# Kernel tuning notes

Hardware: AMD Instinct MI355X
Metric: run time of the kernel (lower is better)

The kernel has to match this reference:

```python
import jax, jax.numpy as jnp
import numpy as np

N_NODES = 100000


def gcn_conv(x, W, b, src, dst, n_nodes):
    """PyG-style GCNConv: add self-loops, symmetric normalization, aggregate to dst."""
    x = x @ W  # [N, out]
    loop = jnp.arange(n_nodes, dtype=src.dtype)
    src_sl = jnp.concatenate([src, loop])  # [E+N]
    dst_sl = jnp.concatenate([dst, loop])
    deg = jax.ops.segment_sum(jnp.ones(src_sl.shape[0], x.dtype), dst_sl,
                              num_segments=n_nodes)  # [N]
    dinv = jnp.where(deg > 0, jax.lax.rsqrt(deg), 0.0)
    norm = dinv[src_sl] * dinv[dst_sl]  # [E+N]
    msg = x[src_sl] * norm[:, None]  # gather + scale
    out = jax.ops.segment_sum(msg, dst_sl, num_segments=n_nodes)  # scatter-add
    return out + b


def setup_inputs() -> dict:
    key = jax.random.key(0)
    ks = jax.random.split(key, 8)
    in_d, hid_d, out_d = 64, 128, 64
    x = jax.random.normal(ks[0], (N_NODES, in_d), dtype=jnp.float32)
    edge_index = jax.random.randint(ks[1], (2, 1000000), 0, N_NODES, dtype=jnp.int64)
    s1 = 1.0 / np.sqrt(in_d)
    s2 = 1.0 / np.sqrt(hid_d)
    sc = 1.0 / np.sqrt(2 * out_d)
    W1 = jax.random.uniform(ks[2], (in_d, hid_d), jnp.float32, -s1, s1)
    b1 = jnp.zeros((hid_d,), jnp.float32)
    W2 = jax.random.uniform(ks[3], (hid_d, out_d), jnp.float32, -s2, s2)
    b2 = jnp.zeros((out_d,), jnp.float32)
    Wc = jax.random.uniform(ks[4], (2 * out_d, 1), jnp.float32, -sc, sc)
    bc = jax.random.uniform(ks[5], (1,), jnp.float32, -sc, sc)
    return {"x": x, "edge_index": edge_index, "W1": W1, "b1": b1,
            "W2": W2, "b2": b2, "Wc": Wc, "bc": bc}


def reference(x, edge_index, W1, b1, W2, b2, Wc, bc):
    src, dst = edge_index[0], edge_index[1]
    h = jax.nn.relu(gcn_conv(x, W1, b1, src, dst, N_NODES))
    h = jax.nn.relu(gcn_conv(h, W2, b2, src, dst, N_NODES))
    # edge-level gather-concat-linear-sigmoid
    edge_emb = jnp.concatenate([h[src], h[dst]], axis=1)  # [E, 2*out_d]
    logits = edge_emb @ Wc + bc  # [E, 1]
    return jax.nn.sigmoid(logits)
```

## Files before the change

### kernel.cpp

```cpp
#include <hip/hip_runtime.h>
#include <hip/hip_fp16.h>
#include <math.h>

#define IN_D 64
#define HID_D 128
#define OUT_D 64

typedef _Float16 half8 __attribute__((ext_vector_type(8)));
typedef float f32x4 __attribute__((ext_vector_type(4)));

#define NBITS  8
#define BNODES 256
#define ECAP   4096
#define CSRCAP (ECAP + BNODES * 7)
#define DCHUNK 2048

__global__ void k_init(int* __restrict__ bcur,
                       const float* __restrict__ W1, const float* __restrict__ W2,
                       __half* __restrict__ w1f, __half* __restrict__ w2f,
                       __half* __restrict__ xs, __half* __restrict__ ts,
                       int N, int nbuk) {
    int t = blockIdx.x * 256 + threadIdx.x;
    if (blockIdx.x == 0) {
        for (int i = threadIdx.x; i < nbuk; i += 256) bcur[i] = i * ECAP;
    }
    if (t < 2048) {
        int which = t >> 10, fl = t & 1023;
        int f = fl >> 6, l = fl & 63, q = l >> 4, n16 = l & 15;
        if (which == 0) {
            int nt = f >> 1, kc = f & 1, n = nt * 16 + n16, k0 = kc * 32 + q * 8;
            for (int j = 0; j < 8; ++j)
                w1f[(size_t)fl * 8 + j] = __float2half(W1[(k0 + j) * 128 + n]);
        } else {
            int nt = f >> 2, kc = f & 3, n = nt * 16 + n16, k0 = kc * 32 + q * 8;
            for (int j = 0; j < 8; ++j)
                w2f[(size_t)fl * 8 + j] = __float2half(W2[(k0 + j) * 64 + n]);
        }
    } else {
        int si = t - 2048;
        if (si < 64) {
            xs[(size_t)N * 64 + si] = __float2half(0.f);
            ts[(size_t)N * 64 + si] = __float2half(0.f);
        }
    }
}

__global__ __launch_bounds__(256) void k_decode3(const unsigned int* __restrict__ raw,
                                                 int E, int nbuk,
                                                 int* __restrict__ bcur,
                                                 int* __restrict__ pairs) {
    __shared__ int hist[512];
    __shared__ int base[512];
    __shared__ int cnt[512];
    __shared__ int is64s;
    if (threadIdx.x == 0) {
        int f = 1;
        for (int i = 1; i < 64; i += 2) f &= (raw[i] == 0u);
        is64s = f;
    }
    for (int i = threadIdx.x; i < nbuk; i += 256) { hist[i] = 0; cnt[i] = 0; }
    __syncthreads();
    int is64 = is64s;
    int e0 = blockIdx.x * DCHUNK;
    int s[8], d[8], b[8];
    if ((E & 1) == 0) {
#pragma unroll
        for (int i = 0; i < 4; ++i) {
            int e = e0 + (threadIdx.x + i * 256) * 2;
            if (e < E) {
                int s0, d0, s1, d1;
                if (is64) {
                    uint4 sv = *(const uint4*)&raw[2 * (size_t)e];
                    uint4 dv = *(const uint4*)&raw[2 * ((size_t)E + e)];
                    s0 = (int)sv.x; s1 = (int)sv.z;
                    d0 = (int)dv.x; d1 = (int)dv.z;
                } else {
                    uint2 sv = *(const uint2*)&raw[e];
                    uint2 dv = *(const uint2*)&raw[E + e];
                    s0 = (int)sv.x; s1 = (int)sv.y;
                    d0 = (int)dv.x; d1 = (int)dv.y;
                }
                s[2 * i] = s0; d[2 * i] = d0; b[2 * i] = d0 >> NBITS;
                s[2 * i + 1] = s1; d[2 * i + 1] = d1; b[2 * i + 1] = d1 >> NBITS;
                atomicAdd(&hist[b[2 * i]], 1);
                atomicAdd(&hist[b[2 * i + 1]], 1);
            } else { b[2 * i] = -1; b[2 * i + 1] = -1; }
        }
    } else {
#pragma unroll
        for (int i = 0; i < 8; ++i) {
            int e = e0 + threadIdx.x + i * 256;
            if (e < E) {
                int sv, dv;
                if (is64) {
                    sv = (int)raw[2 * (size_t)e];
                    dv = (int)raw[2 * ((size_t)E + e)];
                } else {
                    sv = (int)raw[e];
                    dv = (int)raw[E + e];
                }
                s[i] = sv; d[i] = dv; b[i] = dv >> NBITS;
                atomicAdd(&hist[b[i]], 1);
            } else b[i] = -1;
        }
    }
    __syncthreads();
    for (int i = threadIdx.x; i < nbuk; i += 256)
        if (hist[i] > 0) base[i] = atomicAdd(&bcur[i], hist[i]);
    __syncthreads();
#pragma unroll
    for (int i = 0; i < 8; ++i) {
        if (b[i] >= 0) {
            int pos = base[b[i]] + atomicAdd(&cnt[b[i]], 1);
            pairs[pos] = (s[i] << NBITS) | (d[i] & (BNODES - 1));
        }
    }
}

__global__ __launch_bounds__(256) void k_build(const int* __restrict__ pairs,
                                               const int* __restrict__ bcur,
                                               int2* __restrict__ prowdeg,
                                               int* __restrict__ csr_src,
                                               float* __restrict__ dinv,
                                               const float* __restrict__ x,
                                               __half* __restrict__ xs,
                                               int N) {
    __shared__ int deg5[256];
    __shared__ int cur5[256];
    __shared__ int wsum[4];
    int b = blockIdx.x;
    int n0 = b << NBITS;
    int n1 = n0 + BNODES; if (n1 > N) n1 = N;
    int nn = n1 - n0;
    deg5[threadIdx.x] = 0;
    __syncthreads();
    int beg = b * ECAP, end = bcur[b];
    for (int i = beg + threadIdx.x; i < end; i += 256)
        atomicAdd(&deg5[pairs[i] & (BNODES - 1)], 1);
    __syncthreads();
    int pbase = b * CSRCAP;
    int t = threadIdx.x;
    int v0 = deg5[t];
    int p0 = (v0 + 7) & ~7;
    int lane = t & 63, w = t >> 6;
    int inc = p0;
    for (int off = 1; off < 64; off <<= 1) {
        int n = __shfl_up(inc, off);
        if (lane >= off) inc += n;
    }
    if (lane == 63) wsum[w] = inc;
    __syncthreads();
    for (int k = 0; k < w; ++k) inc += wsum[k];
    int ex0 = inc - p0;
    int ps0 = pbase + ex0;
    cur5[t] = ps0;
    if (t < nn) {
        prowdeg[n0 + t] = make_int2(ps0, p0);
        dinv[n0 + t] = rsqrtf((float)v0 + 1.0f);
    }
    __syncthreads();
    for (int i = beg + threadIdx.x; i < end; i += 256) {
        int r = pairs[i];
        int pos = atomicAdd(&cur5[r & (BNODES - 1)], 1);
        csr_src[pos] = r >> NBITS;
    }
    __syncthreads();
    for (int i = cur5[t]; i < ps0 + p0; ++i) csr_src[i] = N;
    for (int idx = t; idx < nn * 8; idx += 256) {
        int i = idx >> 3, c8 = (idx & 7) * 8;
        int node = n0 + i;
        float di = rsqrtf((float)deg5[i] + 1.0f);
        float4 va = *(const float4*)&x[(size_t)node * 64 + c8];
        float4 vb = *(const float4*)&x[(size_t)node * 64 + c8 + 4];
        union { __half2 h[4]; uint4 u; } pk2;
        pk2.h[0] = __floats2half2_rn(va.x * di, va.y * di);
        pk2.h[1] = __floats2half2_rn(va.z * di, va.w * di);
        pk2.h[2] = __floats2half2_rn(vb.x * di, vb.y * di);
        pk2.h[3] = __floats2half2_rn(vb.z * di, vb.w * di);
        *(uint4*)&xs[(size_t)node * 64 + c8] = pk2.u;
    }
}

__global__ __launch_bounds__(256) void k_gather1(const __half* __restrict__ xs,
                          const float* __restrict__ dinv,
                          const int2* __restrict__ prowdeg, const int* __restrict__ csr,
                          __half* __restrict__ agg, int N) {
    int wv = threadIdx.x >> 6, l = threadIdx.x & 63;
    int ns = l >> 4, slot = (l >> 3) & 1, seg = l & 7;
    int node = (blockIdx.x * 4 + wv) * 4 + ns;
    bool valid = node < N;
    int nc = valid ? node : N - 1;
    int2 rp = prowdeg[nc];
    int beg = rp.x;
    int pend = beg + (valid ? rp.y : 0);
    float di = dinv[nc];
    half8 hs = *(const half8*)&xs[(size_t)nc * 64 + seg * 8];
    float acc[8];
#pragma unroll
    for (int j = 0; j < 8; ++j) acc[j] = 0.f;
    for (int k = beg + slot; k < pend; k += 8) {
        int s0 = csr[k], s1 = csr[k + 2], s2 = csr[k + 4], s3 = csr[k + 6];
        half8 h0 = *(const half8*)&xs[(size_t)s0 * 64 + seg * 8];
        half8 h1 = *(const half8*)&xs[(size_t)s1 * 64 + seg * 8];
        half8 h2 = *(const half8*)&xs[(size_t)s2 * 64 + seg * 8];
        half8 h3 = *(const half8*)&xs[(size_t)s3 * 64 + seg * 8];
#pragma unroll
        for (int j = 0; j < 8; ++j) {
            float t01 = (float)h0[j] + (float)h1[j];
            float t23 = (float)h2[j] + (float)h3[j];
            acc[j] += t01 + t23;
        }
    }
#pragma unroll
    for (int j = 0; j < 8; ++j) acc[j] += __shfl_xor(acc[j], 8);
    if (slot == 0 && valid) {
        half8 o;
#pragma unroll
        for (int j = 0; j < 8; ++j) o[j] = (_Float16)((acc[j] + (float)hs[j]) * di);
        *(half8*)&agg[(size_t)node * 64 + seg * 8] = o;
    }
}

__global__ __launch_bounds__(256) void k_gather2(const __half* __restrict__ ts,
                          const float* __restrict__ dinv,
                          const int2* __restrict__ prowdeg, const int* __restrict__ csr,
                          const float* __restrict__ b2, const float* __restrict__ Wc,
                          float* __restrict__ s0o, float* __restrict__ s1o, int N) {
    int wv = threadIdx.x >> 6, l = threadIdx.x & 63;
    int ns = l >> 4, slot = (l >> 3) & 1, seg = l & 7;
    int node = (blockIdx.x * 4 + wv) * 4 + ns;
    bool valid = node < N;
    int nc = valid ? node : N - 1;
    int2 rp = prowdeg[nc];
    int beg = rp.x;
    int pend = beg + (valid ? rp.y : 0);
    float di = dinv[nc];
    half8 hs = *(const half8*)&ts[(size_t)nc * 64 + seg * 8];
    float acc[8];
#pragma unroll
    for (int j = 0; j < 8; ++j) acc[j] = 0.f;
    for (int k = beg + slot; k < pend; k += 8) {
        int s0 = csr[k], s1 = csr[k + 2], s2 = csr[k + 4], s3 = csr[k + 6];
        half8 h0 = *(const half8*)&ts[(size_t)s0 * 64 + seg * 8];
        half8 h1 = *(const half8*)&ts[(size_t)s1 * 64 + seg * 8];
        half8 h2 = *(const half8*)&ts[(size_t)s2 * 64 + seg * 8];
        half8 h3 = *(const half8*)&ts[(size_t)s3 * 64 + seg * 8];
#pragma unroll
        for (int j = 0; j < 8; ++j) {
            float t01 = (float)h0[j] + (float)h1[j];
            float t23 = (float)h2[j] + (float)h3[j];
            acc[j] += t01 + t23;
        }
    }
#pragma unroll
    for (int j = 0; j < 8; ++j) acc[j] += __shfl_xor(acc[j], 8);
    if (slot == 0) {
        float4 b2a = *(const float4*)&b2[seg * 8];
        float4 b2b = *(const float4*)&b2[seg * 8 + 4];
        float4 w0a = *(const float4*)&Wc[seg * 8];
        float4 w0b = *(const float4*)&Wc[seg * 8 + 4];
        float4 w1a = *(const float4*)&Wc[64 + seg * 8];
        float4 w1b = *(const float4*)&Wc[64 + seg * 8 + 4];
        float bb[8] = {b2a.x, b2a.y, b2a.z, b2a.w, b2b.x, b2b.y, b2b.z, b2b.w};
        float w0[8] = {w0a.x, w0a.y, w0a.z, w0a.w, w0b.x, w0b.y, w0b.z, w0b.w};
        float w1[8] = {w1a.x, w1a.y, w1a.z, w1a.w, w1b.x, w1b.y, w1b.z, w1b.w};
        float p0 = 0.f, p1 = 0.f;
#pragma unroll
        for (int j = 0; j < 8; ++j) {
            float v = fmaxf((acc[j] + (float)hs[j]) * di + bb[j], 0.f);
            p0 = fmaf(v, w0[j], p0);
            p1 = fmaf(v, w1[j], p1);
        }
        p0 += __shfl_xor(p0, 1); p1 += __shfl_xor(p1, 1);
        p0 += __shfl_xor(p0, 2); p1 += __shfl_xor(p1, 2);
        p0 += __shfl_xor(p0, 4); p1 += __shfl_xor(p1, 4);
        if (seg == 0 && valid) { s0o[node] = p0; s1o[node] = p1; }
    }
}

__global__ __launch_bounds__(256) void k_mlp_mfma(const __half* __restrict__ agg_h,
                                                  const __half* __restrict__ w1f,
                                                  const __half* __restrict__ w2f,
                                                  const float* __restrict__ b1,
                                                  const float* __restrict__ dinv,
                                                  __half* __restrict__ ts, int N) {
    __shared__ __align__(16) __half w1l[8192];
    __shared__ __align__(16) __half w2l[8192];
    {
        const float4* sA = (const float4*)w1f;
        const float4* sB = (const float4*)w2f;
        float4* dA = (float4*)w1l;
        float4* dB = (float4*)w2l;
        for (int i = threadIdx.x; i < 1024; i += 256) { dA[i] = sA[i]; dB[i] = sB[i]; }
    }
    __syncthreads();

    int wv = threadIdx.x >> 6, l = threadIdx.x & 63;
    int m0 = blockIdx.x * 64 + wv * 16;
    if (m0 >= N) return;
    int q = l >> 4, ml = l & 15;
    int rowA = m0 + ml; if (rowA >= N) rowA = N - 1;

    half8 bfr0 = *(const half8*)&agg_h[(size_t)rowA * 64 + q * 8];
    half8 bfr1 = *(const half8*)&agg_h[(size_t)rowA * 64 + 32 + q * 8];

    int pk[8][2];
#pragma unroll
    for (int nt = 0; nt < 8; ++nt) {
        float4 bb = *(const float4*)&b1[nt * 16 + q * 4];
        f32x4 cacc; cacc[0] = bb.x; cacc[1] = bb.y; cacc[2] = bb.z; cacc[3] = bb.w;
        half8 a0 = *(const half8*)&w1l[(nt * 2 + 0) * 512 + l * 8];
        cacc = __builtin_amdgcn_mfma_f32_16x16x32_f16(a0, bfr0, cacc, 0, 0, 0);
        half8 a1 = *(const half8*)&w1l[(nt * 2 + 1) * 512 + l * 8];
        cacc = __builtin_amdgcn_mfma_f32_16x16x32_f16(a1, bfr1, cacc, 0, 0, 0);
        union { __half2 h; int i; } u0, u1;
        u0.h = __floats2half2_rn(fmaxf(cacc[0], 0.f), fmaxf(cacc[1], 0.f));
        u1.h = __floats2half2_rn(fmaxf(cacc[2], 0.f), fmaxf(cacc[3], 0.f));
        pk[nt][0] = u0.i;
        pk[nt][1] = u1.i;
    }

    int src0 = ml + 16 * ((2 * q) & 3);
    int src1 = ml + 16 * ((2 * q + 1) & 3);
    bool hi = (q >= 2);
    half8 afr[4];
#pragma unroll
    for (int kc = 0; kc < 4; ++kc) {
        int t0 = 2 * kc, t1 = 2 * kc + 1;
        int d0a = __shfl(pk[t0][0], src0), d0b = __shfl(pk[t1][0], src0);
        int d1a = __shfl(pk[t0][1], src0), d1b = __shfl(pk[t1][1], src0);
        int d2a = __shfl(pk[t0][0], src1), d2b = __shfl(pk[t1][0], src1);
        int d3a = __shfl(pk[t0][1], src1), d3b = __shfl(pk[t1][1], src1);
        union { int d[4]; half8 h; } u;
        u.d[0] = hi ? d0b : d0a;
        u.d[1] = hi ? d1b : d1a;
        u.d[2] = hi ? d2b : d2a;
        u.d[3] = hi ? d3b : d3a;
        afr[kc] = u.h;
    }

    float dl = dinv[rowA];
    float dv[4];
#pragma unroll
    for (int r = 0; r < 4; ++r) dv[r] = __shfl(dl, q * 4 + r);

#pragma unroll
    for (int nt2 = 0; nt2 < 4; ++nt2) {
        f32x4 cacc; cacc[0] = 0.f; cacc[1] = 0.f; cacc[2] = 0.f; cacc[3] = 0.f;
#pragma unroll
        for (int kc = 0; kc < 4; ++kc) {
            half8 b = *(const half8*)&w2l[(nt2 * 4 + kc) * 512 + l * 8];
            cacc = __builtin_amdgcn_mfma_f32_16x16x32_f16(afr[kc], b, cacc, 0, 0, 0);
        }
#pragma unroll
        for (int r = 0; r < 4; ++r) {
            int node = m0 + q * 4 + r;
            if (node < N)
                ts[(size_t)node * 64 + nt2 * 16 + ml] = __float2half(cacc[r] * dv[r]);
        }
    }
}

__global__ void k_edge(const unsigned int* __restrict__ raw,
                       const float* __restrict__ s0, const float* __restrict__ s1,
                       const float* __restrict__ bc, float* __restrict__ out, int E) {
    __shared__ int is64s;
    if (threadIdx.x == 0) {
        int f = 1;
        for (int i = 1; i < 64; i += 2) f &= (raw[i] == 0u);
        is64s = f;
    }
    __syncthreads();
    int is64 = is64s;
    int e = (blockIdx.x * blockDim.x + threadIdx.x) * 2;
    if (e >= E) return;
    float b = bc[0];
    if (((E & 1) == 0) && (e + 1 < E)) {
        int sa, sb, da, db;
        if (is64) {
            uint4 sv = *(const uint4*)&raw[2 * (size_t)e];
            uint4 dv = *(const uint4*)&raw[2 * ((size_t)E + e)];
            sa = (int)sv.x; sb = (int)sv.z;
            da = (int)dv.x; db = (int)dv.z;
        } else {
            uint2 sv = *(const uint2*)&raw[e];
            uint2 dv = *(const uint2*)&raw[E + e];
            sa = (int)sv.x; sb = (int)sv.y;
            da = (int)dv.x; db = (int)dv.y;
        }
        float z0 = s0[sa] + s1[da] + b;
        float z1 = s0[sb] + s1[db] + b;
        float2 o;
        o.x = 1.0f / (1.0f + __expf(-z0));
        o.y = 1.0f / (1.0f + __expf(-z1));
        *(float2*)&out[e] = o;
    } else {
        for (int k = e; k < E && k < e + 2; ++k) {
            int sa, da;
            if (is64) {
                sa = (int)raw[2 * (size_t)k];
                da = (int)raw[2 * ((size_t)E + k)];
            } else {
                sa = (int)raw[k];
                da = (int)raw[E + k];
            }
            float z = s0[sa] + s1[da] + b;
            out[k] = 1.0f / (1.0f + __expf(-z));
        }
    }
}

extern "C" void kernel_launch(void* const* d_in, const int* in_sizes, int n_in,
                              void* d_out, int out_size, void* d_ws, size_t ws_size,
                              hipStream_t stream) {
    const float* x  = (const float*)d_in[0];
    const unsigned int* eidx = (const unsigned int*)d_in[1];
    const float* W1 = (const float*)d_in[2];
    const float* b1 = (const float*)d_in[3];
    const float* W2 = (const float*)d_in[4];
    const float* b2 = (const float*)d_in[5];
    const float* Wc = (const float*)d_in[6];
    const float* bc = (const float*)d_in[7];
    float* out = (float*)d_out;

    int N = in_sizes[0] / IN_D;
    int E = in_sizes[1] / 2;
    int nbuk = (N + BNODES - 1) >> NBITS;
    int nchunk = (E + DCHUNK - 1) / DCHUNK;

    char* p = (char*)d_ws;
    int*   bcur    = (int*)p;    p += 512 * 4;
    int*   csr_src = (int*)p;    p += (size_t)nbuk * CSRCAP * 4;
    float* dinv    = (float*)p;  p += (size_t)N * 4;
    float* s0      = (float*)p;  p += (size_t)N * 4;
    float* s1      = (float*)p;  p += (size_t)N * 4;
    p += 15; p = (char*)((size_t)p & ~(size_t)15);
    int2*  prowdeg = (int2*)p;   p += (size_t)N * 8;
    int*   pairs   = (int*)p;    p += (size_t)nbuk * ECAP * 4;
    __half* xs    = (__half*)p;  p += (size_t)(N + 1) * 64 * 2;
    __half* aggh  = (__half*)p;  p += (size_t)N * 64 * 2;
    __half* ts    = (__half*)p;  p += (size_t)(N + 1) * 64 * 2;
    __half* w1f   = (__half*)p;  p += 8192 * 2;
    __half* w2f   = (__half*)p;  p += 8192 * 2;

    k_init<<<9, 256, 0, stream>>>(bcur, W1, W2, w1f, w2f, xs, ts, N, nbuk);
    k_decode3<<<nchunk, 256, 0, stream>>>(eidx, E, nbuk, bcur, pairs);
    k_build<<<nbuk, 256, 0, stream>>>(pairs, bcur, prowdeg, csr_src, dinv, x, xs, N);

    k_gather1<<<(N + 15) / 16, 256, 0, stream>>>(xs, dinv, prowdeg, csr_src, aggh, N);

    k_mlp_mfma<<<(N + 63) / 64, 256, 0, stream>>>(aggh, w1f, w2f, b1, dinv, ts, N);

    k_gather2<<<(N + 15) / 16, 256, 0, stream>>>(ts, dinv, prowdeg, csr_src,
                                                 b2, Wc, s0, s1, N);

    k_edge<<<(E / 2 + 255) / 256, 256, 0, stream>>>(eidx, s0, s1, bc, out, E);
}
```

Before: 182.1 us.

## Drop init kernel, fold weight prep into build, widen decode chunks

Removes the separate k_init launch. The bucket cursors now start from a memset to zero and bucket offsets are added at use, while the weight-fragment conversion and pad-row zeroing move into the first blocks of k_build. k_decode3 now handles 4096 edges per block, with a uint4 path for 32-bit indices, so fewer blocks issue global atomics and loads are wider. The trade-off is higher register pressure in decode and a few build blocks doing extra work.

```diff
diff --git a/kernel.cpp b/kernel.cpp
--- a/kernel.cpp
+++ b/kernel.cpp
@@ -13,37 +13,7 @@
 #define BNODES 256
 #define ECAP   4096
 #define CSRCAP (ECAP + BNODES * 7)
-#define DCHUNK 2048
-
-__global__ void k_init(int* __restrict__ bcur,
-                       const float* __restrict__ W1, const float* __restrict__ W2,
-                       __half* __restrict__ w1f, __half* __restrict__ w2f,
-                       __half* __restrict__ xs, __half* __restrict__ ts,
-                       int N, int nbuk) {
-    int t = blockIdx.x * 256 + threadIdx.x;
-    if (blockIdx.x == 0) {
-        for (int i = threadIdx.x; i < nbuk; i += 256) bcur[i] = i * ECAP;
-    }
-    if (t < 2048) {
-        int which = t >> 10, fl = t & 1023;
-        int f = fl >> 6, l = fl & 63, q = l >> 4, n16 = l & 15;
-        if (which == 0) {
-            int nt = f >> 1, kc = f & 1, n = nt * 16 + n16, k0 = kc * 32 + q * 8;
-            for (int j = 0; j < 8; ++j)
-                w1f[(size_t)fl * 8 + j] = __float2half(W1[(k0 + j) * 128 + n]);
-        } else {
-            int nt = f >> 2, kc = f & 3, n = nt * 16 + n16, k0 = kc * 32 + q * 8;
-            for (int j = 0; j < 8; ++j)
-                w2f[(size_t)fl * 8 + j] = __float2half(W2[(k0 + j) * 64 + n]);
-        }
-    } else {
-        int si = t - 2048;
-        if (si < 64) {
-            xs[(size_t)N * 64 + si] = __float2half(0.f);
-            ts[(size_t)N * 64 + si] = __float2half(0.f);
-        }
-    }
-}
+#define DCHUNK 4096
 
 __global__ __launch_bounds__(256) void k_decode3(const unsigned int* __restrict__ raw,
                                                  int E, int nbuk,
@@ -62,33 +32,45 @@
     __syncthreads();
     int is64 = is64s;
     int e0 = blockIdx.x * DCHUNK;
-    int s[8], d[8], b[8];
-    if ((E & 1) == 0) {
+    int s[16], d[16], b[16];
+    if ((E & 3) == 0 && !is64) {
 #pragma unroll
         for (int i = 0; i < 4; ++i) {
+            int e = e0 + (threadIdx.x + i * 256) * 4;
+            if (e < E) {
+                uint4 sv = *(const uint4*)&raw[e];
+                uint4 dv = *(const uint4*)&raw[E + e];
+                int ss[4] = {(int)sv.x, (int)sv.y, (int)sv.z, (int)sv.w};
+                int dd[4] = {(int)dv.x, (int)dv.y, (int)dv.z, (int)dv.w};
+#pragma unroll
+                for (int j = 0; j < 4; ++j) {
+                    s[4 * i + j] = ss[j]; d[4 * i + j] = dd[j];
+                    b[4 * i + j] = dd[j] >> NBITS;
+                    atomicAdd(&hist[b[4 * i + j]], 1);
+                }
+            } else {
+#pragma unroll
+                for (int j = 0; j < 4; ++j) b[4 * i + j] = -1;
+            }
+        }
+    } else if ((E & 1) == 0 && is64) {
+#pragma unroll
+        for (int i = 0; i < 8; ++i) {
             int e = e0 + (threadIdx.x + i * 256) * 2;
             if (e < E) {
-                int s0, d0, s1, d1;
-                if (is64) {
-                    uint4 sv = *(const uint4*)&raw[2 * (size_t)e];
-                    uint4 dv = *(const uint4*)&raw[2 * ((size_t)E + e)];
-                    s0 = (int)sv.x; s1 = (int)sv.z;
-                    d0 = (int)dv.x; d1 = (int)dv.z;
-                } else {
-                    uint2 sv = *(const uint2*)&raw[e];
-                    uint2 dv = *(const uint2*)&raw[E + e];
-                    s0 = (int)sv.x; s1 = (int)sv.y;
-                    d0 = (int)dv.x; d1 = (int)dv.y;
-                }
-                s[2 * i] = s0; d[2 * i] = d0; b[2 * i] = d0 >> NBITS;
-                s[2 * i + 1] = s1; d[2 * i + 1] = d1; b[2 * i + 1] = d1 >> NBITS;
+                uint4 sv = *(const uint4*)&raw[2 * (size_t)e];
+                uint4 dv = *(const uint4*)&raw[2 * ((size_t)E + e)];
+                s[2 * i] = (int)sv.x; s[2 * i + 1] = (int)sv.z;
+                d[2 * i] = (int)dv.x; d[2 * i + 1] = (int)dv.z;
+                b[2 * i] = d[2 * i] >> NBITS;
+                b[2 * i + 1] = d[2 * i + 1] >> NBITS;
                 atomicAdd(&hist[b[2 * i]], 1);
                 atomicAdd(&hist[b[2 * i + 1]], 1);
             } else { b[2 * i] = -1; b[2 * i + 1] = -1; }
         }
     } else {
 #pragma unroll
-        for (int i = 0; i < 8; ++i) {
+        for (int i = 0; i < 16; ++i) {
             int e = e0 + threadIdx.x + i * 256;
             if (e < E) {
                 int sv, dv;
@@ -106,10 +88,10 @@
     }
     __syncthreads();
     for (int i = threadIdx.x; i < nbuk; i += 256)
-        if (hist[i] > 0) base[i] = atomicAdd(&bcur[i], hist[i]);
-    __syncthreads();
-#pragma unroll
-    for (int i = 0; i < 8; ++i) {
+        if (hist[i] > 0) base[i] = i * ECAP + atomicAdd(&bcur[i], hist[i]);
+    __syncthreads();
+#pragma unroll
+    for (int i = 0; i < 16; ++i) {
         if (b[i] >= 0) {
             int pos = base[b[i]] + atomicAdd(&cnt[b[i]], 1);
             pairs[pos] = (s[i] << NBITS) | (d[i] & (BNODES - 1));
@@ -124,17 +106,43 @@
                                                float* __restrict__ dinv,
                                                const float* __restrict__ x,
                                                __half* __restrict__ xs,
+                                               const float* __restrict__ W1,
+                                               const float* __restrict__ W2,
+                                               __half* __restrict__ w1f,
+                                               __half* __restrict__ w2f,
+                                               __half* __restrict__ ts,
                                                int N) {
     __shared__ int deg5[256];
     __shared__ int cur5[256];
     __shared__ int wsum[4];
     int b = blockIdx.x;
+    if (b < 9) {
+        int t = b * 256 + threadIdx.x;
+        if (t < 2048) {
+            int which = t >> 10, fl = t & 1023;
+            int f = fl >> 6, l = fl & 63, q = l >> 4, n16 = l & 15;
+            if (which == 0) {
+                int nt = f >> 1, kc = f & 1, n = nt * 16 + n16, k0 = kc * 32 + q * 8;
+                for (int j = 0; j < 8; ++j)
+                    w1f[(size_t)fl * 8 + j] = __float2half(W1[(k0 + j) * 128 + n]);
+            } else {
+                int nt = f >> 2, kc = f & 3, n = nt * 16 + n16, k0 = kc * 32 + q * 8;
+                for (int j = 0; j < 8; ++j)
+                    w2f[(size_t)fl * 8 + j] = __float2half(W2[(k0 + j) * 64 + n]);
+            }
+        }
+    } else if (b == 9) {
+        if (threadIdx.x < 64) {
+            xs[(size_t)N * 64 + threadIdx.x] = __float2half(0.f);
+            ts[(size_t)N * 64 + threadIdx.x] = __float2half(0.f);
+        }
+    }
     int n0 = b << NBITS;
     int n1 = n0 + BNODES; if (n1 > N) n1 = N;
     int nn = n1 - n0;
     deg5[threadIdx.x] = 0;
     __syncthreads();
-    int beg = b * ECAP, end = bcur[b];
+    int beg = b * ECAP, end = beg + bcur[b];
     for (int i = beg + threadIdx.x; i < end; i += 256)
         atomicAdd(&deg5[pairs[i] & (BNODES - 1)], 1);
     __syncthreads();
@@ -443,9 +451,11 @@
     __half* w1f   = (__half*)p;  p += 8192 * 2;
     __half* w2f   = (__half*)p;  p += 8192 * 2;
 
-    k_init<<<9, 256, 0, stream>>>(bcur, W1, W2, w1f, w2f, xs, ts, N, nbuk);
+    hipMemsetAsync(bcur, 0, 512 * 4, stream);
+
     k_decode3<<<nchunk, 256, 0, stream>>>(eidx, E, nbuk, bcur, pairs);
-    k_build<<<nbuk, 256, 0, stream>>>(pairs, bcur, prowdeg, csr_src, dinv, x, xs, N);
+    k_build<<<nbuk, 256, 0, stream>>>(pairs, bcur, prowdeg, csr_src, dinv,
+                                      x, xs, W1, W2, w1f, w2f, ts, N);
 
     k_gather1<<<(N + 15) / 16, 256, 0, stream>>>(xs, dinv, prowdeg, csr_src, aggh, N);
 
```

Result: faster. 178.2 us (-2.1%).
